# Optimization experiments

Measured on AMD Instinct MI355X. Metric: run time of the kernel, lower is better.

The kernel has to match this reference:

```python
import jax, jax.numpy as jnp
import numpy as np

N = 200000      # nodes (Elliptic-like AML graph)
E = 400000      # edges
F_IN = 165      # num_features
H = 512         # hidden_units
C = 2           # num_classes


def setup_inputs() -> dict:
    key = jax.random.key(0)
    ks = jax.random.split(key, 10)

    def glorot(k, shape):
        fan_in = shape[0]
        return (jax.random.normal(k, shape, jnp.float32) / np.float32(np.sqrt(fan_in)))

    return {
        "x": jax.random.normal(ks[0], (N, F_IN), jnp.float32),
        "edge_index": jax.random.randint(ks[1], (2, E), 0, N, dtype=jnp.int32),
        # ChebConv1: K=2 -> two weight mats + one bias
        "W1_0": glorot(ks[2], (F_IN, H)),
        "W1_1": glorot(ks[3], (F_IN, H)),
        "b1": jnp.zeros((H,), jnp.float32),
        # ChebConv2: K=2
        "W2_0": glorot(ks[4], (H, H)),
        "W2_1": glorot(ks[5], (H, H)),
        "b2": jnp.zeros((H,), jnp.float32),
        # final Linear
        "Wl": glorot(ks[6], (H, C)),
        "bl": jnp.zeros((C,), jnp.float32),
    }


def _edge_norm(src, dst, n, dtype):
    # Scaled Chebyshev Laplacian L_hat = 2L/lambda_max - I with sym norm and
    # lambda_max=2 (PyG defaults): diagonal is 0, off-diag = -D^{-1/2} A D^{-1/2}.
    ones = jnp.ones(src.shape[0], dtype)
    deg = jax.ops.segment_sum(ones, src, num_segments=n)
    dis = jnp.where(deg > 0, jax.lax.rsqrt(jnp.where(deg > 0, deg, 1.0)), 0.0)
    return -dis[src] * dis[dst]  # [E]


def _prop(h, src, dst, w, n):
    # One application of L_hat: gather -> weight -> scatter-add. [E, F] messages.
    return jax.ops.segment_sum(w[:, None] * h[src], dst, num_segments=n)


def reference(x, edge_index, W1_0, W1_1, b1, W2_0, W2_1, b2, Wl, bl):
    n = x.shape[0]
    src, dst = edge_index[0], edge_index[1]
    w = _edge_norm(src, dst, n, x.dtype)
    # ChebConv K=2: out = Tx0 @ W0 + Tx1 @ W1 + b, Tx1 = L_hat x
    h = jax.nn.relu(x @ W1_0 + _prop(x, src, dst, w, n) @ W1_1 + b1)
    h = jax.nn.relu(h @ W2_0 + _prop(h, src, dst, w, n) @ W2_1 + b2)
    return h @ Wl + bl  # [N, C] logits
```

## Files before the change

### kernel.cpp

```cpp
#include <hip/hip_runtime.h>

#define NNODES 200000
#define MPAD   200064
#define NEDGES 400000
#define FIN    165
#define K1P    192
#define HID    512
#define NB     ((NNODES + 255) / 256)

typedef __bf16 bf16_t;
typedef __bf16 bf16x8 __attribute__((ext_vector_type(8)));
typedef float  f32x4  __attribute__((ext_vector_type(4)));
typedef unsigned short su16x8 __attribute__((ext_vector_type(8)));
typedef float f32x4u __attribute__((ext_vector_type(4), aligned(4)));

static __device__ __forceinline__ float bf2f(unsigned short u) {
    unsigned int x = ((unsigned int)u) << 16;
    return __builtin_bit_cast(float, x);
}
static __device__ __forceinline__ unsigned short f2bf(float f) {
    bf16_t h = (bf16_t)f;
    return __builtin_bit_cast(unsigned short, h);
}
static __device__ __forceinline__ void gl_lds16(const void* g, void* l) {
    __builtin_amdgcn_global_load_lds(
        (const __attribute__((address_space(1))) unsigned int*)g,
        (__attribute__((address_space(3))) unsigned int*)l, 16, 0, 0);
}
static __device__ __forceinline__ int xcd_swz(int i, int nb) {
    int q = nb >> 3, r = nb & 7;
    int xcd = i & 7, seq = i >> 3;
    return (xcd < r ? xcd * (q + 1) : r * (q + 1) + (xcd - r) * q) + seq;
}

__global__ void k_deg(const int* __restrict__ src, const int* __restrict__ dst,
                      int* __restrict__ deg, int* __restrict__ cnt, int E) {
    int e = blockIdx.x * 256 + threadIdx.x;
    if (e < E) {
        atomicAdd(&deg[src[e]], 1);
        atomicAdd(&cnt[dst[e]], 1);
    }
}

__global__ void k_scan1(int* __restrict__ cnt, int* __restrict__ btot, int n) {
    __shared__ int s[256];
    int i = blockIdx.x * 256 + threadIdx.x;
    int v = (i < n) ? cnt[i] : 0;
    s[threadIdx.x] = v;
    __syncthreads();
    #pragma unroll
    for (int off = 1; off < 256; off <<= 1) {
        int t = (threadIdx.x >= off) ? s[threadIdx.x - off] : 0;
        __syncthreads();
        s[threadIdx.x] += t;
        __syncthreads();
    }
    if (i < n) cnt[i] = s[threadIdx.x] - v;
    if (threadIdx.x == 255) btot[blockIdx.x] = s[255];
}

__global__ void k_scan2(int* __restrict__ btot, int nb) {
    __shared__ int s[1024];
    int i = threadIdx.x;
    int v = (i < nb) ? btot[i] : 0;
    s[i] = v;
    __syncthreads();
    #pragma unroll
    for (int off = 1; off < 1024; off <<= 1) {
        int t = (i >= off) ? s[i - off] : 0;
        __syncthreads();
        s[i] += t;
        __syncthreads();
    }
    if (i < nb) btot[i] = s[i] - v;
}

__global__ void k_scan3(int* __restrict__ cnt, const int* __restrict__ btot,
                        int* __restrict__ rowptr, int n, int E) {
    int i = blockIdx.x * 256 + threadIdx.x;
    if (i < n) {
        rowptr[i] = cnt[i] + btot[blockIdx.x];
        cnt[i] = 0;
    }
    if (i == 0) rowptr[n] = E;
}

__global__ void k_scatter(const int* __restrict__ src, const int* __restrict__ dst,
                          const int* __restrict__ rowptr, int* __restrict__ cur,
                          const int* __restrict__ deg, int* __restrict__ esrc,
                          float* __restrict__ ew, int E) {
    int e = blockIdx.x * 256 + threadIdx.x;
    if (e < E) {
        int s = src[e], d = dst[e];
        int pos = rowptr[d] + atomicAdd(&cur[d], 1);
        esrc[pos] = s;
        if (ew) {
            int da = deg[s], db = deg[d];
            float fa = da > 0 ? rsqrtf((float)da) : 0.f;
            float fb = db > 0 ? rsqrtf((float)db) : 0.f;
            ew[pos] = -fa * fb;
        }
    }
}

__global__ void k_buildP(const float* __restrict__ W, unsigned short* __restrict__ P,
                         int kp, int kfull) {
    int idx = blockIdx.x * 256 + threadIdx.x;
    if (idx >= kp * HID) return;
    int j  = idx & 7;
    int n  = (idx >> 3) & 511;
    int q  = (idx >> 12) & 3;
    int kt = idx >> 14;
    int k  = kt * 32 + q * 8 + j;
    P[idx] = (k < kfull) ? f2bf(W[(size_t)k * HID + n]) : (unsigned short)0;
}

__global__ void k_buildP2cat(const float* __restrict__ W0, const float* __restrict__ W1,
                             unsigned short* __restrict__ P) {
    int idx = blockIdx.x * 256 + threadIdx.x;
    if (idx >= 1024 * HID) return;
    int j  = idx & 7;
    int n  = (idx >> 3) & 511;
    int q  = (idx >> 12) & 3;
    int kt = idx >> 14;
    int k  = kt * 32 + q * 8 + j;
    float v = (k < HID) ? W0[(size_t)k * HID + n] : W1[(size_t)(k - HID) * HID + n];
    P[idx] = f2bf(v);
}

__global__ void k_xcvt(const float* __restrict__ x, unsigned short* __restrict__ xb) {
    long i = ((long)blockIdx.x * 256 + threadIdx.x) * 8;
    if (i >= (long)NNODES * K1P) return;
    int row = (int)(i / K1P), k = (int)(i % K1P);
    const float* xr = x + (size_t)row * FIN;
    __align__(16) unsigned short v[8];
    #pragma unroll
    for (int j = 0; j < 8; ++j)
        v[j] = (k + j < FIN) ? f2bf(xr[k + j]) : (unsigned short)0;
    *(su16x8*)&xb[i] = *(su16x8*)v;
}

template<int K, int LDA, int NCMB>
__global__ __launch_bounds__(256, 4)
void k_gemms(const unsigned short* __restrict__ A, const unsigned short* __restrict__ P,
             unsigned short* __restrict__ D0, unsigned short* __restrict__ D1,
             int os0, int os1, int ob0, int ob1) {
    constexpr int KT = K / 32;
    __shared__ unsigned short Al[128 * 32];
    __shared__ unsigned short Bl[4 * 128 * 8];

    const int t    = threadIdx.x;
    const int lane = t & 63;
    const int wv   = t >> 6;
    const int wm   = wv >> 1, wn = wv & 1;
    const int wg   = xcd_swz(blockIdx.x, gridDim.x);
    const int combo = wg & (NCMB - 1);
    const int sel  = combo >> 2;
    const int ncol = (combo & 3) * 128;
    const int m0   = (wg / NCMB) * 128;
    const unsigned short* Pb = P + (size_t)sel * K * 512 + ncol * 8;
    unsigned short* D = sel ? D1 : D0;
    const int os = sel ? os1 : os0;
    const int oc = (sel ? ob1 : ob0) + ncol;

    const int arow = t >> 2, ach = t & 3;
    const unsigned short* Ab = A + (size_t)m0 * LDA;

    f32x4 acc[4][4];
    #pragma unroll
    for (int m = 0; m < 4; ++m)
        #pragma unroll
        for (int n = 0; n < 4; ++n)
            acc[m][n] = (f32x4){0.f, 0.f, 0.f, 0.f};

    for (int kt = 0; kt < KT; ++kt) {
        __syncthreads();
        #pragma unroll
        for (int i = 0; i < 2; ++i) {
            int r = arow + i * 64;
            gl_lds16(Ab + (size_t)r * LDA + kt * 32 + (ach ^ ((r >> 1) & 3)) * 8,
                     &Al[t * 8 + i * 2048]);
        }
        #pragma unroll
        for (int i = 0; i < 2; ++i)
            gl_lds16(Pb + (size_t)kt * 16384 + wv * 4096 + lane * 8 + i * 512,
                     &Bl[wv * 1024 + lane * 8 + i * 512]);
        __syncthreads();

        bf16x8 af[4], bfr[4];
        const int kq = lane >> 4;
        #pragma unroll
        for (int m = 0; m < 4; ++m) {
            int r = wm * 64 + m * 16 + (lane & 15);
            af[m] = *(const bf16x8*)&Al[r * 32 + 8 * (kq ^ ((r >> 1) & 3))];
        }
        #pragma unroll
        for (int n = 0; n < 4; ++n) {
            int c = wn * 64 + n * 16 + (lane & 15);
            bfr[n] = *(const bf16x8*)&Bl[kq * 1024 + c * 8];
        }
        #pragma unroll
        for (int m = 0; m < 4; ++m)
            #pragma unroll
            for (int n = 0; n < 4; ++n)
                acc[m][n] = __builtin_amdgcn_mfma_f32_16x16x32_bf16(bfr[n], af[m], acc[m][n], 0, 0, 0);
    }

    #pragma unroll
    for (int m = 0; m < 4; ++m) {
        int r = m0 + wm * 64 + m * 16 + (lane & 15);
        #pragma unroll
        for (int n = 0; n < 4; ++n) {
            int cb = oc + wn * 64 + n * 16 + (lane >> 4) * 4;
            uint2 pk;
            pk.x = ((unsigned int)f2bf(acc[m][n][1]) << 16) | (unsigned int)f2bf(acc[m][n][0]);
            pk.y = ((unsigned int)f2bf(acc[m][n][3]) << 16) | (unsigned int)f2bf(acc[m][n][2]);
            *(uint2*)&D[(size_t)r * os + cb] = pk;
        }
    }
}

__global__ __launch_bounds__(256, 4)
void k_gemmf(const unsigned short* __restrict__ A, const unsigned short* __restrict__ P,
             const float* __restrict__ b2, const float* __restrict__ Wl,
             float* __restrict__ out) {
    constexpr int K = 1024, LDA = 1024, KT = K / 32;
    __shared__ unsigned short Al[128 * 32];
    __shared__ unsigned short Bl[4 * 128 * 8];

    const int t    = threadIdx.x;
    const int lane = t & 63;
    const int wv   = t >> 6;
    const int wm   = wv >> 1, wn = wv & 1;
    const int wg   = xcd_swz(blockIdx.x, gridDim.x);
    const int ncol = (wg & 3) * 128;
    const int m0   = (wg >> 2) * 128;
    const unsigned short* Pb = P + ncol * 8;
    const int arow = t >> 2, ach = t & 3;
    const unsigned short* Ab = A + (size_t)m0 * LDA;

    f32x4 acc[4][4];
    #pragma unroll
    for (int m = 0; m < 4; ++m)
        #pragma unroll
        for (int n = 0; n < 4; ++n)
            acc[m][n] = (f32x4){0.f, 0.f, 0.f, 0.f};

    for (int kt = 0; kt < KT; ++kt) {
        __syncthreads();
        #pragma unroll
        for (int i = 0; i < 2; ++i) {
            int r = arow + i * 64;
            gl_lds16(Ab + (size_t)r * LDA + kt * 32 + (ach ^ ((r >> 1) & 3)) * 8,
                     &Al[t * 8 + i * 2048]);
        }
        #pragma unroll
        for (int i = 0; i < 2; ++i)
            gl_lds16(Pb + (size_t)kt * 16384 + wv * 4096 + lane * 8 + i * 512,
                     &Bl[wv * 1024 + lane * 8 + i * 512]);
        __syncthreads();

        bf16x8 af[4], bfr[4];
        const int kq = lane >> 4;
        #pragma unroll
        for (int m = 0; m < 4; ++m) {
            int r = wm * 64 + m * 16 + (lane & 15);
            af[m] = *(const bf16x8*)&Al[r * 32 + 8 * (kq ^ ((r >> 1) & 3))];
        }
        #pragma unroll
        for (int n = 0; n < 4; ++n) {
            int c = wn * 64 + n * 16 + (lane & 15);
            bfr[n] = *(const bf16x8*)&Bl[kq * 1024 + c * 8];
        }
        #pragma unroll
        for (int m = 0; m < 4; ++m)
            #pragma unroll
            for (int n = 0; n < 4; ++n)
                acc[m][n] = __builtin_amdgcn_mfma_f32_16x16x32_bf16(bfr[n], af[m], acc[m][n], 0, 0, 0);
    }

    float s0[4] = {0.f, 0.f, 0.f, 0.f}, s1[4] = {0.f, 0.f, 0.f, 0.f};
    #pragma unroll
    for (int n = 0; n < 4; ++n) {
        int cg = ncol + wn * 64 + n * 16 + (lane >> 4) * 4;
        float4 bb   = *(const float4*)(b2 + cg);
        float4 wl01 = *(const float4*)(Wl + (size_t)cg * 2);
        float4 wl23 = *(const float4*)(Wl + (size_t)cg * 2 + 4);
        float b2v[4] = {bb.x, bb.y, bb.z, bb.w};
        float w0v[4] = {wl01.x, wl01.z, wl23.x, wl23.z};
        float w1v[4] = {wl01.y, wl01.w, wl23.y, wl23.w};
        #pragma unroll
        for (int m = 0; m < 4; ++m)
            #pragma unroll
            for (int j = 0; j < 4; ++j) {
                float z = acc[m][n][j] + b2v[j];
                z = z > 0.f ? z : 0.f;
                s0[m] += z * w0v[j];
                s1[m] += z * w1v[j];
            }
    }
    #pragma unroll
    for (int m = 0; m < 4; ++m) {
        s0[m] += __shfl_xor(s0[m], 16, 64);
        s0[m] += __shfl_xor(s0[m], 32, 64);
        s1[m] += __shfl_xor(s1[m], 16, 64);
        s1[m] += __shfl_xor(s1[m], 32, 64);
    }
    if (lane < 16) {
        #pragma unroll
        for (int m = 0; m < 4; ++m) {
            int r = m0 + wm * 64 + m * 16 + lane;
            if (r < NNODES) {
                unsafeAtomicAdd(&out[2 * (size_t)r],     s0[m]);
                unsafeAtomicAdd(&out[2 * (size_t)r + 1], s1[m]);
            }
        }
    }
}

__global__ void k_initout(float* __restrict__ out, const float* __restrict__ bl, int M) {
    int i = blockIdx.x * 256 + threadIdx.x;
    if (i < 2 * M) out[i] = bl[i & 1];
}

__global__ __launch_bounds__(512, 1)
void k_gemmw(const unsigned short* __restrict__ A, const unsigned short* __restrict__ P,
             unsigned short* __restrict__ U, int ooff, int M) {
    constexpr int KT = HID / 32;
    __shared__ unsigned short Al[2][128 * 32];
    __shared__ unsigned short Bl[2][4][HID * 8];

    const int t    = threadIdx.x;
    const int lane = t & 63;
    const int wv   = t >> 6;
    const int wm   = wv >> 2, wn = wv & 3;
    const int m0   = blockIdx.x * 128;

    const int srow = t >> 2;
    const int gch  = ((t & 3) ^ ((srow >> 1) & 3)) * 8;
    const unsigned short* Ab = A + (size_t)(m0 + srow) * 1024 + gch;
    const bool rok = (m0 + srow) < M;
    const unsigned short* Pb = P + (size_t)t * 8;

    f32x4 acc[4][8];
    #pragma unroll
    for (int m = 0; m < 4; ++m)
        #pragma unroll
        for (int n = 0; n < 8; ++n)
            acc[m][n] = (f32x4){0.f, 0.f, 0.f, 0.f};

    if (rok) gl_lds16(Ab, &Al[0][t * 8]);
    #pragma unroll
    for (int q = 0; q < 4; ++q) gl_lds16(Pb + q * 4096, &Bl[0][q][t * 8]);
    __syncthreads();

    int cur = 0;
    for (int kt = 0; kt < KT; ++kt) {
        if (kt + 1 < KT) {
            if (rok) gl_lds16(Ab + (kt + 1) * 32, &Al[cur ^ 1][t * 8]);
            const unsigned short* Pn = Pb + (size_t)(kt + 1) * 16384;
            #pragma unroll
            for (int q = 0; q < 4; ++q)
                gl_lds16(Pn + q * 4096, &Bl[cur ^ 1][q][t * 8]);
        }
        bf16x8 af[4], bfr[8];
        #pragma unroll
        for (int m = 0; m < 4; ++m) {
            int r  = wm * 64 + m * 16 + (lane & 15);
            int kq = lane >> 4;
            af[m] = *(const bf16x8*)&Al[cur][r * 32 + 8 * (kq ^ ((r >> 1) & 3))];
        }
        #pragma unroll
        for (int n = 0; n < 8; ++n) {
            int c = wn * 128 + n * 16 + (lane & 15);
            bfr[n] = *(const bf16x8*)&Bl[cur][lane >> 4][c * 8];
        }
        #pragma unroll
        for (int m = 0; m < 4; ++m)
            #pragma unroll
            for (int n = 0; n < 8; ++n)
                acc[m][n] = __builtin_amdgcn_mfma_f32_16x16x32_bf16(bfr[n], af[m], acc[m][n], 0, 0, 0);
        __syncthreads();
        cur ^= 1;
    }

    #pragma unroll
    for (int m = 0; m < 4; ++m) {
        int r = m0 + wm * 64 + m * 16 + (lane & 15);
        if (r < M) {
            #pragma unroll
            for (int n = 0; n < 8; ++n) {
                int cb = ooff + wn * 128 + n * 16 + (lane >> 4) * 4;
                uint2 pk;
                pk.x = ((unsigned int)f2bf(acc[m][n][1]) << 16) | (unsigned int)f2bf(acc[m][n][0]);
                pk.y = ((unsigned int)f2bf(acc[m][n][3]) << 16) | (unsigned int)f2bf(acc[m][n][2]);
                *(uint2*)&U[(size_t)r * 1024 + cb] = pk;
            }
        }
    }
}

__global__ __launch_bounds__(512, 1)
void k_gemm0(const float* __restrict__ Aptr, const unsigned short* __restrict__ P,
             unsigned short* __restrict__ U, int ooff, int M) {
    constexpr int K  = K1P;
    constexpr int KT = K / 32;
    __shared__ unsigned short Al[128 * 32];
    __shared__ unsigned short Bpl[4][HID * 8];

    const int t    = threadIdx.x;
    const int lane = t & 63;
    const int wv   = t >> 6;
    const int wm   = wv >> 2, wn = wv & 3;
    const int m0   = blockIdx.x * 128;

    f32x4 acc[4][8];
    #pragma unroll
    for (int m = 0; m < 4; ++m)
        #pragma unroll
        for (int n = 0; n < 8; ++n)
            acc[m][n] = (f32x4){0.f, 0.f, 0.f, 0.f};

    const int srow = t >> 2, sch = t & 3;
    const bool rok = (m0 + srow) < M;

    for (int kt = 0; kt < KT; ++kt) {
        const int k0 = kt * 32;
        __syncthreads();
        {
            const int gk = k0 + sch * 8;
            su16x8 av;
            float f[8];
            const float* Ab = Aptr + (size_t)(m0 + srow) * FIN + gk;
            if (rok && gk + 8 <= FIN) {
                f32x4u lo = *(const f32x4u*)Ab;
                f32x4u hi = *(const f32x4u*)(Ab + 4);
                f[0]=lo.x; f[1]=lo.y; f[2]=lo.z; f[3]=lo.w;
                f[4]=hi.x; f[5]=hi.y; f[6]=hi.z; f[7]=hi.w;
            } else {
                #pragma unroll
                for (int j = 0; j < 8; ++j)
                    f[j] = (rok && gk + j < FIN) ? Ab[j] : 0.f;
            }
            #pragma unroll
            for (int j = 0; j < 8; ++j) av[j] = f2bf(f[j]);
            *(su16x8*)&Al[srow * 32 + 8 * (sch ^ ((srow >> 1) & 3))] = av;
        }
        {
            const unsigned short* Pb = P + (size_t)kt * 16384 + t * 8;
            #pragma unroll
            for (int q = 0; q < 4; ++q)
                *(su16x8*)&Bpl[q][t * 8] = *(const su16x8*)(Pb + q * 4096);
        }
        __syncthreads();
        bf16x8 af[4], bfr[8];
        #pragma unroll
        for (int m = 0; m < 4; ++m) {
            int r  = wm * 64 + m * 16 + (lane & 15);
            int kq = lane >> 4;
            af[m] = *(const bf16x8*)&Al[r * 32 + 8 * (kq ^ ((r >> 1) & 3))];
        }
        #pragma unroll
        for (int n = 0; n < 8; ++n) {
            int c = wn * 128 + n * 16 + (lane & 15);
            bfr[n] = *(const bf16x8*)&Bpl[lane >> 4][c * 8];
        }
        #pragma unroll
        for (int m = 0; m < 4; ++m)
            #pragma unroll
            for (int n = 0; n < 8; ++n)
                acc[m][n] = __builtin_amdgcn_mfma_f32_16x16x32_bf16(bfr[n], af[m], acc[m][n], 0, 0, 0);
    }

    #pragma unroll
    for (int m = 0; m < 4; ++m) {
        int r = m0 + wm * 64 + m * 16 + (lane & 15);
        if (r < M) {
            #pragma unroll
            for (int n = 0; n < 8; ++n) {
                int cb = ooff + wn * 128 + n * 16 + (lane >> 4) * 4;
                uint2 pk;
                pk.x = ((unsigned int)f2bf(acc[m][n][1]) << 16) | (unsigned int)f2bf(acc[m][n][0]);
                pk.y = ((unsigned int)f2bf(acc[m][n][3]) << 16) | (unsigned int)f2bf(acc[m][n][2]);
                *(uint2*)&U[(size_t)r * 1024 + cb] = pk;
            }
        }
    }
}

template<int RELU, int HASW>
__global__ void k_aggr(unsigned short* U, const int* __restrict__ rowptr,
                       const int* __restrict__ esrc, const float* __restrict__ ew,
                       const int* __restrict__ deg, const float* __restrict__ bias, int M) {
    int wid  = (blockIdx.x * 256 + threadIdx.x) >> 6;
    int lane = threadIdx.x & 63;
    if (wid >= M) return;
    int e0 = rowptr[wid], e1 = rowptr[wid + 1];
    if (RELU == 0 && e0 == e1) return;

    unsigned short* u0 = U + (size_t)wid * 1024 + lane * 8;
    uint4 v0 = *(const uint4*)u0;
    unsigned int a0[4] = {v0.x, v0.y, v0.z, v0.w};
    float acc[8], ac2[8];
    #pragma unroll
    for (int i = 0; i < 4; ++i) {
        acc[2 * i]     = bf2f((unsigned short)(a0[i] & 0xffffu));
        acc[2 * i + 1] = bf2f((unsigned short)(a0[i] >> 16));
        ac2[2 * i] = 0.f; ac2[2 * i + 1] = 0.f;
    }

    float dr = 0.f;
    if (!HASW && e0 < e1) {
        int dd = deg[wid];
        dr = dd > 0 ? rsqrtf((float)dd) : 0.f;
    }
    int e = e0;
    for (; e + 1 < e1; e += 2) {
        int sa = esrc[e], sb = esrc[e + 1];
        float wa = HASW ? ew[e]     : -dr * rsqrtf((float)deg[sa]);
        float wb = HASW ? ew[e + 1] : -dr * rsqrtf((float)deg[sb]);
        const uint4 va = *(const uint4*)(U + (size_t)sa * 1024 + 512 + lane * 8);
        const uint4 vb = *(const uint4*)(U + (size_t)sb * 1024 + 512 + lane * 8);
        unsigned int ua[4] = {va.x, va.y, va.z, va.w};
        unsigned int ub[4] = {vb.x, vb.y, vb.z, vb.w};
        #pragma unroll
        for (int i = 0; i < 4; ++i) {
            acc[2 * i]     += wa * bf2f((unsigned short)(ua[i] & 0xffffu));
            acc[2 * i + 1] += wa * bf2f((unsigned short)(ua[i] >> 16));
            ac2[2 * i]     += wb * bf2f((unsigned short)(ub[i] & 0xffffu));
            ac2[2 * i + 1] += wb * bf2f((unsigned short)(ub[i] >> 16));
        }
    }
    if (e < e1) {
        int sa = esrc[e];
        float wa = HASW ? ew[e] : -dr * rsqrtf((float)deg[sa]);
        const uint4 va = *(const uint4*)(U + (size_t)sa * 1024 + 512 + lane * 8);
        unsigned int ua[4] = {va.x, va.y, va.z, va.w};
        #pragma unroll
        for (int i = 0; i < 4; ++i) {
            acc[2 * i]     += wa * bf2f((unsigned short)(ua[i] & 0xffffu));
            acc[2 * i + 1] += wa * bf2f((unsigned short)(ua[i] >> 16));
        }
    }
    #pragma unroll
    for (int i = 0; i < 8; ++i) acc[i] += ac2[i];

    if (RELU) {
        float4 c0 = *(const float4*)(bias + lane * 8);
        float4 c1 = *(const float4*)(bias + lane * 8 + 4);
        float bb[8] = {c0.x,c0.y,c0.z,c0.w,c1.x,c1.y,c1.z,c1.w};
        #pragma unroll
        for (int i = 0; i < 8; ++i) {
            float f = acc[i] + bb[i];
            acc[i] = f > 0.f ? f : 0.f;
        }
    }
    uint4 w4;
    unsigned int* wo = (unsigned int*)&w4;
    #pragma unroll
    for (int i = 0; i < 4; ++i)
        wo[i] = ((unsigned int)f2bf(acc[2 * i + 1]) << 16) | (unsigned int)f2bf(acc[2 * i]);
    *(uint4*)u0 = w4;
}

__global__ void k_aggr2(unsigned short* U, const int* __restrict__ rowptr,
                        const int* __restrict__ esrc, const float* __restrict__ ew, int M) {
    int wid  = (blockIdx.x * 256 + threadIdx.x) >> 6;
    int lane = threadIdx.x & 63;
    if (wid >= M) return;
    int e0 = rowptr[wid], e1 = rowptr[wid + 1];

    float acc[8] = {0.f,0.f,0.f,0.f,0.f,0.f,0.f,0.f};
    float ac2[8] = {0.f,0.f,0.f,0.f,0.f,0.f,0.f,0.f};
    int e = e0;
    for (; e + 1 < e1; e += 2) {
        int sa = esrc[e], sb = esrc[e + 1];
        float wa = ew[e], wb = ew[e + 1];
        const uint4 va = *(const uint4*)(U + (size_t)sa * 1024 + lane * 8);
        const uint4 vb = *(const uint4*)(U + (size_t)sb * 1024 + lane * 8);
        unsigned int ua[4] = {va.x, va.y, va.z, va.w};
        unsigned int ub[4] = {vb.x, vb.y, vb.z, vb.w};
        #pragma unroll
        for (int i = 0; i < 4; ++i) {
            acc[2 * i]     += wa * bf2f((unsigned short)(ua[i] & 0xffffu));
            acc[2 * i + 1] += wa * bf2f((unsigned short)(ua[i] >> 16));
            ac2[2 * i]     += wb * bf2f((unsigned short)(ub[i] & 0xffffu));
            ac2[2 * i + 1] += wb * bf2f((unsigned short)(ub[i] >> 16));
        }
    }
    if (e < e1) {
        int sa = esrc[e];
        float wa = ew[e];
        const uint4 va = *(const uint4*)(U + (size_t)sa * 1024 + lane * 8);
        unsigned int ua[4] = {va.x, va.y, va.z, va.w};
        #pragma unroll
        for (int i = 0; i < 4; ++i) {
            acc[2 * i]     += wa * bf2f((unsigned short)(ua[i] & 0xffffu));
            acc[2 * i + 1] += wa * bf2f((unsigned short)(ua[i] >> 16));
        }
    }
    uint4 w4;
    unsigned int* wo = (unsigned int*)&w4;
    #pragma unroll
    for (int i = 0; i < 4; ++i)
        wo[i] = ((unsigned int)f2bf(acc[2 * i + 1] + ac2[2 * i + 1]) << 16) |
                 (unsigned int)f2bf(acc[2 * i] + ac2[2 * i]);
    *(uint4*)(U + (size_t)wid * 1024 + 512 + lane * 8) = w4;
}

__global__ void k_final(const unsigned short* __restrict__ U, const float* __restrict__ b2,
                        const float* __restrict__ Wl, const float* __restrict__ bl,
                        float* __restrict__ out, int M) {
    int wid  = (blockIdx.x * 256 + threadIdx.x) >> 6;
    int lane = threadIdx.x & 63;
    if (wid >= M) return;
    const uint4 v = *(const uint4*)(U + (size_t)wid * 1024 + lane * 8);
    float4 c0 = *(const float4*)(b2 + lane * 8);
    float4 c1 = *(const float4*)(b2 + lane * 8 + 4);
    float bb[8] = {c0.x,c0.y,c0.z,c0.w,c1.x,c1.y,c1.z,c1.w};
    const float4* Wp = reinterpret_cast<const float4*>(Wl + lane * 16);
    float4 w0 = Wp[0], w1 = Wp[1], w2 = Wp[2], w3 = Wp[3];
    float wv[16] = {w0.x, w0.y, w0.z, w0.w, w1.x, w1.y, w1.z, w1.w,
                    w2.x, w2.y, w2.z, w2.w, w3.x, w3.y, w3.z, w3.w};
    unsigned int uu[4] = {v.x, v.y, v.z, v.w};
    float s0 = 0.f, s1 = 0.f;
    #pragma unroll
    for (int j = 0; j < 4; ++j) {
        float f0 = bf2f((unsigned short)(uu[j] & 0xffffu)) + bb[2 * j];
        float f1 = bf2f((unsigned short)(uu[j] >> 16))     + bb[2 * j + 1];
        f0 = f0 > 0.f ? f0 : 0.f;
        f1 = f1 > 0.f ? f1 : 0.f;
        s0 += f0 * wv[4 * j + 0];
        s1 += f0 * wv[4 * j + 1];
        s0 += f1 * wv[4 * j + 2];
        s1 += f1 * wv[4 * j + 3];
    }
    #pragma unroll
    for (int off = 32; off; off >>= 1) {
        s0 += __shfl_xor(s0, off, 64);
        s1 += __shfl_xor(s1, off, 64);
    }
    if (lane == 0) {
        out[2 * (size_t)wid]     = s0 + bl[0];
        out[2 * (size_t)wid + 1] = s1 + bl[1];
    }
}

extern "C" void kernel_launch(void* const* d_in, const int* in_sizes, int n_in,
                              void* d_out, int out_size, void* d_ws, size_t ws_size,
                              hipStream_t stream) {
    const float* x    = (const float*)d_in[0];
    const int*   ei   = (const int*)d_in[1];
    const float* W1_0 = (const float*)d_in[2];
    const float* W1_1 = (const float*)d_in[3];
    const float* b1   = (const float*)d_in[4];
    const float* W2_0 = (const float*)d_in[5];
    const float* W2_1 = (const float*)d_in[6];
    const float* b2   = (const float*)d_in[7];
    const float* Wl   = (const float*)d_in[8];
    const float* bl   = (const float*)d_in[9];
    const int* src = ei;
    const int* dst = ei + NEDGES;
    float* out = (float*)d_out;

    char* ws = (char*)d_ws;
    size_t off = 0;
    auto alloc = [&](size_t bytes) -> void* {
        void* p = ws + off;
        off += (bytes + 255) & ~(size_t)255;
        return p;
    };
    int*            deg    = (int*)alloc((size_t)NNODES * 4);
    int*            cnt    = (int*)alloc((size_t)NNODES * 4);
    int*            rowptr = (int*)alloc((size_t)(NNODES + 1) * 4);
    int*            btot   = (int*)alloc((size_t)NB * 4);
    unsigned short* P1     = (unsigned short*)alloc((size_t)2 * K1P * HID * 2);
    unsigned short* P2     = (unsigned short*)alloc((size_t)2 * HID * HID * 2);
    unsigned short* U      = (unsigned short*)alloc((size_t)MPAD * 1024 * 2);

    bool esrc_ws = (off + (size_t)NEDGES * 8 <= ws_size);
    int*   esrc = esrc_ws ? (int*)alloc((size_t)NEDGES * 4)   : (int*)d_out;
    float* ew   = esrc_ws ? (float*)alloc((size_t)NEDGES * 4) : nullptr;
    bool have_xb = (off + (size_t)MPAD * K1P * 2 <= ws_size);
    unsigned short* xb = have_xb ? (unsigned short*)alloc((size_t)MPAD * K1P * 2) : nullptr;

    hipMemsetAsync(deg, 0, (size_t)NNODES * 4, stream);
    hipMemsetAsync(cnt, 0, (size_t)NNODES * 4, stream);

    k_deg    <<<(NEDGES + 255) / 256, 256, 0, stream>>>(src, dst, deg, cnt, NEDGES);
    k_scan1  <<<NB, 256, 0, stream>>>(cnt, btot, NNODES);
    k_scan2  <<<1, 1024, 0, stream>>>(btot, NB);
    k_scan3  <<<NB, 256, 0, stream>>>(cnt, btot, rowptr, NNODES, NEDGES);
    k_scatter<<<(NEDGES + 255) / 256, 256, 0, stream>>>(src, dst, rowptr, cnt, deg,
                                                        esrc, ew, NEDGES);

    const int pg1 = (K1P * HID + 255) / 256, pg2 = (HID * HID + 255) / 256;
    k_buildP<<<pg1, 256, 0, stream>>>(W1_0, P1, K1P, FIN);
    k_buildP<<<pg1, 256, 0, stream>>>(W1_1, P1 + (size_t)K1P * HID, K1P, FIN);
    if (esrc_ws) {
        k_buildP2cat<<<(1024 * HID + 255) / 256, 256, 0, stream>>>(W2_0, W2_1, P2);
    } else {
        k_buildP<<<pg2, 256, 0, stream>>>(W2_0, P2, HID, HID);
        k_buildP<<<pg2, 256, 0, stream>>>(W2_1, P2 + (size_t)HID * HID, HID, HID);
    }

    const int nblk = MPAD / 128;

    if (have_xb) {
        k_xcvt<<<(int)(((long)NNODES * K1P / 8 + 255) / 256), 256, 0, stream>>>(x, xb);
        k_gemms<K1P, K1P, 8><<<8 * nblk, 256, 0, stream>>>(xb, P1, U, U, 1024, 1024, 0, 512);
    } else {
        k_gemm0<<<nblk, 512, 0, stream>>>(x, P1, U, 0, NNODES);
        k_gemm0<<<nblk, 512, 0, stream>>>(x, P1 + (size_t)K1P * HID, U, 512, NNODES);
    }

    if (esrc_ws) {
        k_aggr<1, 1><<<NNODES / 4, 256, 0, stream>>>(U, rowptr, esrc, ew, deg, b1, NNODES);
        k_aggr2<<<NNODES / 4, 256, 0, stream>>>(U, rowptr, esrc, ew, NNODES);
        k_initout<<<(2 * NNODES + 255) / 256, 256, 0, stream>>>(out, bl, NNODES);
        k_gemmf<<<4 * nblk, 256, 0, stream>>>(U, P2, b2, Wl, out);
    } else {
        k_aggr<1, 0><<<NNODES / 4, 256, 0, stream>>>(U, rowptr, esrc, nullptr, deg, b1, NNODES);
        k_gemms<HID, 1024, 4><<<4 * nblk, 256, 0, stream>>>(U, P2 + (size_t)HID * HID,
                                                            U, U, 1024, 1024, 512, 512);
        k_gemmw<<<nblk, 512, 0, stream>>>(U, P2, U, 0, NNODES);
        k_aggr<0, 0><<<NNODES / 4, 256, 0, stream>>>(U, rowptr, esrc, nullptr, deg, nullptr, NNODES);
        k_final<<<NNODES / 4, 256, 0, stream>>>(U, b2, Wl, bl, out, NNODES);
    }
}
```

Before: 808.4 us.

## Double K-step per LDS stage in GEMMs and fold small init kernels

The two MFMA GEMM kernels now stage a 64-wide K slice per iteration instead of 32, with a new XOR swizzle over eight 16-byte chunks. This halves the number of barrier pairs and load rounds per tile and raises LDS use per block. Output bias initialisation is folded into the edge scatter kernel, which works because E equals 2N. The two layer-1 weight packing launches are merged into one, cutting kernel launches.

```diff
diff --git a/kernel.cpp b/kernel.cpp
--- a/kernel.cpp
+++ b/kernel.cpp
@@ -88,7 +88,8 @@
 __global__ void k_scatter(const int* __restrict__ src, const int* __restrict__ dst,
                           const int* __restrict__ rowptr, int* __restrict__ cur,
                           const int* __restrict__ deg, int* __restrict__ esrc,
-                          float* __restrict__ ew, int E) {
+                          float* __restrict__ ew, float* __restrict__ outinit,
+                          const float* __restrict__ bl, int E) {
     int e = blockIdx.x * 256 + threadIdx.x;
     if (e < E) {
         int s = src[e], d = dst[e];
@@ -100,7 +101,23 @@
             float fb = db > 0 ? rsqrtf((float)db) : 0.f;
             ew[pos] = -fa * fb;
         }
-    }
+        if (outinit) outinit[e] = bl[e & 1];
+    }
+}
+
+__global__ void k_buildP1(const float* __restrict__ W0, const float* __restrict__ W1,
+                          unsigned short* __restrict__ P) {
+    int idx = blockIdx.x * 256 + threadIdx.x;
+    if (idx >= 2 * K1P * HID) return;
+    int panel = idx / (K1P * HID);
+    int rem   = idx - panel * (K1P * HID);
+    int j  = rem & 7;
+    int n  = (rem >> 3) & 511;
+    int q  = (rem >> 12) & 3;
+    int kt = rem >> 14;
+    int k  = kt * 32 + q * 8 + j;
+    const float* W = panel ? W1 : W0;
+    P[idx] = (k < FIN) ? f2bf(W[(size_t)k * HID + n]) : (unsigned short)0;
 }
 
 __global__ void k_buildP(const float* __restrict__ W, unsigned short* __restrict__ P,
@@ -140,14 +157,15 @@
     *(su16x8*)&xb[i] = *(su16x8*)v;
 }
 
+
 template<int K, int LDA, int NCMB>
 __global__ __launch_bounds__(256, 4)
 void k_gemms(const unsigned short* __restrict__ A, const unsigned short* __restrict__ P,
              unsigned short* __restrict__ D0, unsigned short* __restrict__ D1,
              int os0, int os1, int ob0, int ob1) {
-    constexpr int KT = K / 32;
-    __shared__ unsigned short Al[128 * 32];
-    __shared__ unsigned short Bl[4 * 128 * 8];
+    constexpr int KT2 = K / 64;
+    __shared__ unsigned short Al[128 * 64];
+    __shared__ unsigned short Bl[2][4][1024];
 
     const int t    = threadIdx.x;
     const int lane = t & 63;
@@ -163,8 +181,9 @@
     const int os = sel ? os1 : os0;
     const int oc = (sel ? ob1 : ob0) + ncol;
 
-    const int arow = t >> 2, ach = t & 3;
     const unsigned short* Ab = A + (size_t)m0 * LDA;
+    const int ar0 = t >> 3;
+    const int ach = t & 7;
 
     f32x4 acc[4][4];
     #pragma unroll
@@ -173,37 +192,43 @@
         for (int n = 0; n < 4; ++n)
             acc[m][n] = (f32x4){0.f, 0.f, 0.f, 0.f};
 
-    for (int kt = 0; kt < KT; ++kt) {
-        __syncthreads();
-        #pragma unroll
-        for (int i = 0; i < 2; ++i) {
-            int r = arow + i * 64;
-            gl_lds16(Ab + (size_t)r * LDA + kt * 32 + (ach ^ ((r >> 1) & 3)) * 8,
-                     &Al[t * 8 + i * 2048]);
-        }
-        #pragma unroll
-        for (int i = 0; i < 2; ++i)
-            gl_lds16(Pb + (size_t)kt * 16384 + wv * 4096 + lane * 8 + i * 512,
-                     &Bl[wv * 1024 + lane * 8 + i * 512]);
-        __syncthreads();
-
-        bf16x8 af[4], bfr[4];
+    for (int kt = 0; kt < KT2; ++kt) {
+        __syncthreads();
+        #pragma unroll
+        for (int i = 0; i < 4; ++i) {
+            int r = i * 32 + ar0;
+            gl_lds16(Ab + (size_t)r * LDA + kt * 64 + (ach ^ (r & 7)) * 8,
+                     &Al[i * 2048 + t * 8]);
+        }
+        #pragma unroll
+        for (int h = 0; h < 2; ++h)
+            #pragma unroll
+            for (int i = 0; i < 2; ++i)
+                gl_lds16(Pb + (size_t)(kt * 2 + h) * 16384 + wv * 4096 + lane * 8 + i * 512,
+                         &Bl[h][wv][lane * 8 + i * 512]);
+        __syncthreads();
+
         const int kq = lane >> 4;
         #pragma unroll
-        for (int m = 0; m < 4; ++m) {
-            int r = wm * 64 + m * 16 + (lane & 15);
-            af[m] = *(const bf16x8*)&Al[r * 32 + 8 * (kq ^ ((r >> 1) & 3))];
-        }
-        #pragma unroll
-        for (int n = 0; n < 4; ++n) {
-            int c = wn * 64 + n * 16 + (lane & 15);
-            bfr[n] = *(const bf16x8*)&Bl[kq * 1024 + c * 8];
-        }
-        #pragma unroll
-        for (int m = 0; m < 4; ++m)
-            #pragma unroll
-            for (int n = 0; n < 4; ++n)
-                acc[m][n] = __builtin_amdgcn_mfma_f32_16x16x32_bf16(bfr[n], af[m], acc[m][n], 0, 0, 0);
+        for (int ks = 0; ks < 2; ++ks) {
+            bf16x8 af[4], bfr[4];
+            #pragma unroll
+            for (int m = 0; m < 4; ++m) {
+                int r = wm * 64 + m * 16 + (lane & 15);
+                int c = ks * 4 + kq;
+                af[m] = *(const bf16x8*)&Al[r * 64 + (c ^ (r & 7)) * 8];
+            }
+            #pragma unroll
+            for (int n = 0; n < 4; ++n) {
+                int c = wn * 64 + n * 16 + (lane & 15);
+                bfr[n] = *(const bf16x8*)&Bl[ks][kq][c * 8];
+            }
+            #pragma unroll
+            for (int m = 0; m < 4; ++m)
+                #pragma unroll
+                for (int n = 0; n < 4; ++n)
+                    acc[m][n] = __builtin_amdgcn_mfma_f32_16x16x32_bf16(bfr[n], af[m], acc[m][n], 0, 0, 0);
+        }
     }
 
     #pragma unroll
@@ -224,9 +249,9 @@
 void k_gemmf(const unsigned short* __restrict__ A, const unsigned short* __restrict__ P,
              const float* __restrict__ b2, const float* __restrict__ Wl,
              float* __restrict__ out) {
-    constexpr int K = 1024, LDA = 1024, KT = K / 32;
-    __shared__ unsigned short Al[128 * 32];
-    __shared__ unsigned short Bl[4 * 128 * 8];
+    constexpr int K = 1024, LDA = 1024, KT2 = K / 64;
+    __shared__ unsigned short Al[128 * 64];
+    __shared__ unsigned short Bl[2][4][1024];
 
     const int t    = threadIdx.x;
     const int lane = t & 63;
@@ -236,8 +261,8 @@
     const int ncol = (wg & 3) * 128;
     const int m0   = (wg >> 2) * 128;
     const unsigned short* Pb = P + ncol * 8;
-    const int arow = t >> 2, ach = t & 3;
     const unsigned short* Ab = A + (size_t)m0 * LDA;
+    const int ar0 = t >> 3, ach = t & 7;
 
     f32x4 acc[4][4];
     #pragma unroll
@@ -246,37 +271,43 @@
         for (int n = 0; n < 4; ++n)
             acc[m][n] = (f32x4){0.f, 0.f, 0.f, 0.f};
 
-    for (int kt = 0; kt < KT; ++kt) {
-        __syncthreads();
-        #pragma unroll
-        for (int i = 0; i < 2; ++i) {
-            int r = arow + i * 64;
-            gl_lds16(Ab + (size_t)r * LDA + kt * 32 + (ach ^ ((r >> 1) & 3)) * 8,
-                     &Al[t * 8 + i * 2048]);
-        }
-        #pragma unroll
-        for (int i = 0; i < 2; ++i)
-            gl_lds16(Pb + (size_t)kt * 16384 + wv * 4096 + lane * 8 + i * 512,
-                     &Bl[wv * 1024 + lane * 8 + i * 512]);
-        __syncthreads();
-
-        bf16x8 af[4], bfr[4];
+    for (int kt = 0; kt < KT2; ++kt) {
+        __syncthreads();
+        #pragma unroll
+        for (int i = 0; i < 4; ++i) {
+            int r = i * 32 + ar0;
+            gl_lds16(Ab + (size_t)r * LDA + kt * 64 + (ach ^ (r & 7)) * 8,
+                     &Al[i * 2048 + t * 8]);
+        }
+        #pragma unroll
+        for (int h = 0; h < 2; ++h)
+            #pragma unroll
+            for (int i = 0; i < 2; ++i)
+                gl_lds16(Pb + (size_t)(kt * 2 + h) * 16384 + wv * 4096 + lane * 8 + i * 512,
+                         &Bl[h][wv][lane * 8 + i * 512]);
+        __syncthreads();
+
         const int kq = lane >> 4;
         #pragma unroll
-        for (int m = 0; m < 4; ++m) {
-            int r = wm * 64 + m * 16 + (lane & 15);
-            af[m] = *(const bf16x8*)&Al[r * 32 + 8 * (kq ^ ((r >> 1) & 3))];
-        }
-        #pragma unroll
-        for (int n = 0; n < 4; ++n) {
-            int c = wn * 64 + n * 16 + (lane & 15);
-            bfr[n] = *(const bf16x8*)&Bl[kq * 1024 + c * 8];
-        }
-        #pragma unroll
-        for (int m = 0; m < 4; ++m)
-            #pragma unroll
-            for (int n = 0; n < 4; ++n)
-                acc[m][n] = __builtin_amdgcn_mfma_f32_16x16x32_bf16(bfr[n], af[m], acc[m][n], 0, 0, 0);
+        for (int ks = 0; ks < 2; ++ks) {
+            bf16x8 af[4], bfr[4];
+            #pragma unroll
+            for (int m = 0; m < 4; ++m) {
+                int r = wm * 64 + m * 16 + (lane & 15);
+                int c = ks * 4 + kq;
+                af[m] = *(const bf16x8*)&Al[r * 64 + (c ^ (r & 7)) * 8];
+            }
+            #pragma unroll
+            for (int n = 0; n < 4; ++n) {
+                int c = wn * 64 + n * 16 + (lane & 15);
+                bfr[n] = *(const bf16x8*)&Bl[ks][kq][c * 8];
+            }
+            #pragma unroll
+            for (int m = 0; m < 4; ++m)
+                #pragma unroll
+                for (int n = 0; n < 4; ++n)
+                    acc[m][n] = __builtin_amdgcn_mfma_f32_16x16x32_bf16(bfr[n], af[m], acc[m][n], 0, 0, 0);
+        }
     }
 
     float s0[4] = {0.f, 0.f, 0.f, 0.f}, s1[4] = {0.f, 0.f, 0.f, 0.f};
@@ -316,11 +347,6 @@
             }
         }
     }
-}
-
-__global__ void k_initout(float* __restrict__ out, const float* __restrict__ bl, int M) {
-    int i = blockIdx.x * 256 + threadIdx.x;
-    if (i < 2 * M) out[i] = bl[i & 1];
 }
 
 __global__ __launch_bounds__(512, 1)
@@ -691,15 +717,14 @@
     k_scan1  <<<NB, 256, 0, stream>>>(cnt, btot, NNODES);
     k_scan2  <<<1, 1024, 0, stream>>>(btot, NB);
     k_scan3  <<<NB, 256, 0, stream>>>(cnt, btot, rowptr, NNODES, NEDGES);
-    k_scatter<<<(NEDGES + 255) / 256, 256, 0, stream>>>(src, dst, rowptr, cnt, deg,
-                                                        esrc, ew, NEDGES);
-
-    const int pg1 = (K1P * HID + 255) / 256, pg2 = (HID * HID + 255) / 256;
-    k_buildP<<<pg1, 256, 0, stream>>>(W1_0, P1, K1P, FIN);
-    k_buildP<<<pg1, 256, 0, stream>>>(W1_1, P1 + (size_t)K1P * HID, K1P, FIN);
+    k_scatter<<<(NEDGES + 255) / 256, 256, 0, stream>>>(src, dst, rowptr, cnt, deg, esrc,
+                                                        ew, esrc_ws ? out : nullptr, bl, NEDGES);
+
+    k_buildP1<<<(2 * K1P * HID + 255) / 256, 256, 0, stream>>>(W1_0, W1_1, P1);
     if (esrc_ws) {
         k_buildP2cat<<<(1024 * HID + 255) / 256, 256, 0, stream>>>(W2_0, W2_1, P2);
     } else {
+        const int pg2 = (HID * HID + 255) / 256;
         k_buildP<<<pg2, 256, 0, stream>>>(W2_0, P2, HID, HID);
         k_buildP<<<pg2, 256, 0, stream>>>(W2_1, P2 + (size_t)HID * HID, HID, HID);
     }
@@ -717,7 +742,6 @@
     if (esrc_ws) {
         k_aggr<1, 1><<<NNODES / 4, 256, 0, stream>>>(U, rowptr, esrc, ew, deg, b1, NNODES);
         k_aggr2<<<NNODES / 4, 256, 0, stream>>>(U, rowptr, esrc, ew, NNODES);
-        k_initout<<<(2 * NNODES + 255) / 256, 256, 0, stream>>>(out, bl, NNODES);
         k_gemmf<<<4 * nblk, 256, 0, stream>>>(U, P2, b2, Wl, out);
     } else {
         k_aggr<1, 0><<<NNODES / 4, 256, 0, stream>>>(U, rowptr, esrc, nullptr, deg, b1, NNODES);
```

After: 777.5 us. 1.04x faster.
